# Performance work log

Hardware: AMD Instinct MI355X
Metric: run time of the kernel (lower is better)

Reference implementation:

```python
import math
import jax, jax.numpy as jnp
import numpy as np

H, KV, D = 16, 4, 128          # num_heads, num_kv_heads, head_dim
HID = 2048                      # hidden_size
ROPE_BASE = 1e6
EPS = 1e-6


def setup_inputs() -> dict:
    key = jax.random.key(0)
    ks = jax.random.split(key, 3)
    B, S = 2, 2048
    s = 0.02
    return {
        "x": jax.random.normal(ks[0], (B, S, HID), jnp.float32),
        "w_qkv": jax.random.normal(ks[1], (2 * H * D + 2 * KV * D, HID), jnp.float32) * s,
        "w_o": jax.random.normal(ks[2], (HID, H * D), jnp.float32) * s,
        "q_norm_w": jnp.ones((D,), jnp.float32),
        "q_norm_b": jnp.zeros((D,), jnp.float32),
        "k_norm_w": jnp.ones((D,), jnp.float32),
        "k_norm_b": jnp.zeros((D,), jnp.float32),
    }


def _layernorm(x, w, b):
    mu = jnp.mean(x, axis=-1, keepdims=True)
    xc = x - mu
    var = jnp.mean(xc * xc, axis=-1, keepdims=True)
    return xc * jax.lax.rsqrt(var + EPS) * w + b


def _rope(x, cos, sin):
    # x: [B, h, S, D]; cos/sin: [S, D/2]; interleaved real/imag pairs
    xr, xi = x[..., 0::2], x[..., 1::2]
    c, s = cos[None, None], sin[None, None]
    out = jnp.stack([xr * c - xi * s, xr * s + xi * c], axis=-1)
    return out.reshape(x.shape)


def reference(x, w_qkv, w_o, q_norm_w, q_norm_b, k_norm_w, k_norm_b):
    B, S, _ = x.shape
    qkv = x @ w_qkv.T                                  # [B,S,2*H*D+2*KV*D]
    qg, k, v = jnp.split(qkv, [2 * H * D, 2 * H * D + KV * D], axis=-1)
    q, gate = jnp.split(qg, 2, axis=-1)                # [B,S,H*D] each

    q = q.reshape(B, S, H, D).transpose(0, 2, 1, 3)    # [B,H,S,D]
    k = k.reshape(B, S, KV, D).transpose(0, 2, 1, 3)   # [B,KV,S,D]
    v = v.reshape(B, S, KV, D).transpose(0, 2, 1, 3)

    q = _layernorm(q, q_norm_w, q_norm_b)
    k = _layernorm(k, k_norm_w, k_norm_b)

    inv = 1.0 / (ROPE_BASE ** (jnp.arange(0, D, 2, dtype=jnp.float32) / D))
    freqs = jnp.outer(jnp.arange(S, dtype=jnp.float32), inv)  # [S, D/2]
    cos, sin = jnp.cos(freqs), jnp.sin(freqs)
    q = _rope(q, cos, sin)
    k = _rope(k, cos, sin)

    rep = H // KV
    k = jnp.repeat(k, rep, axis=1)                     # [B,H,S,D]
    v = jnp.repeat(v, rep, axis=1)

    scores = jnp.einsum('bhqd,bhkd->bhqk', q, k) / math.sqrt(D)
    causal = jnp.tril(jnp.ones((S, S), bool))
    scores = jnp.where(causal[None, None], scores, -jnp.inf)
    attn = jax.nn.softmax(scores, axis=-1)
    out = jnp.einsum('bhqk,bhkd->bhqd', attn, v)
    out = out.transpose(0, 2, 1, 3).reshape(B, S, H * D)
    out = out * jax.nn.sigmoid(gate)
    return out @ w_o.T
```

## Files before the change

### kernel.cpp

```cpp
#include <hip/hip_runtime.h>
#include <hip/hip_bf16.h>

typedef __bf16 bf16_t;
typedef __bf16 bf16x2 __attribute__((ext_vector_type(2)));
typedef __bf16 bf16x4v __attribute__((ext_vector_type(4)));
typedef __bf16 bf16x8 __attribute__((ext_vector_type(8)));
typedef float f32x4 __attribute__((ext_vector_type(4)));

#define LOG2E 1.4426950408889634f
#define QSCALE (0.08838834764831843f * 1.4426950408889634f)

__global__ __launch_bounds__(256) void cvt_f32_bf16(const float* __restrict__ in,
                                                    bf16_t* __restrict__ out, int n4) {
  int i = blockIdx.x * 256 + threadIdx.x;
  if (i < n4) {
    float4 v = ((const float4*)in)[i];
    bf16x4v o;
    o[0] = (__bf16)v.x; o[1] = (__bf16)v.y; o[2] = (__bf16)v.z; o[3] = (__bf16)v.w;
    *(bf16x4v*)(out + (size_t)i * 4) = o;
  }
}

__global__ __launch_bounds__(256) void rope_tables(float* __restrict__ cosT,
                                                   float* __restrict__ sinT) {
  int idx = blockIdx.x * 256 + threadIdx.x;
  int s = idx >> 6, i = idx & 63;
  float inv = __builtin_amdgcn_exp2f(-(float)i * (19.931568569324174f / 64.0f));
  float f = (float)s * inv;
  cosT[idx] = cosf(f);
  sinT[idx] = sinf(f);
}

template<int MI, int NI, typename OT>
__global__ __launch_bounds__(512) void gemm8p(const bf16_t* __restrict__ A,
                                              const bf16_t* __restrict__ B,
                                              OT* __restrict__ C,
                                              int M, int N, int K) {
  constexpr int BM = MI * 32;
  constexpr int BN = NI * 64;
  constexpr int NA = BM / 64;
  constexpr int NB = BN / 64;
  constexpr int ST = NA + NB;

  __shared__ bf16_t LA[2][BM * 64];
  __shared__ bf16_t LB[2][BN * 64];

  int nb = N / BN;
  int cpx = gridDim.x >> 3;
  int bid = blockIdx.x;
  int swz = (bid & 7) * cpx + (bid >> 3);
  int bm = swz / nb, bn = swz % nb;
  int m0 = bm * BM, n0 = bn * BN;
  int tid = threadIdx.x, lane = tid & 63, wv = tid >> 6;
  int wr = wv >> 2, wc = wv & 3, lr = lane & 15, g = lane >> 4;
  int T = K >> 6;

  auto stageI = [&](int kt, int bi, int s) {
    int k0 = kt << 6;
    if (s < NA) {
      int c = s * 512 + tid;
      int row = c >> 3, lc = (c & 7) ^ (row & 7);
      __builtin_amdgcn_global_load_lds(
          (const __attribute__((address_space(1))) void*)(A + (size_t)(m0 + row) * K + k0 + lc * 8),
          (__attribute__((address_space(3))) void*)&LA[bi][(s * 512 + wv * 64) * 8], 16, 0, 0);
    } else {
      int c = (s - NA) * 512 + tid;
      int row = c >> 3, lc = (c & 7) ^ (row & 7);
      __builtin_amdgcn_global_load_lds(
          (const __attribute__((address_space(1))) void*)(B + (size_t)(n0 + row) * K + k0 + lc * 8),
          (__attribute__((address_space(3))) void*)&LB[bi][((s - NA) * 512 + wv * 64) * 8], 16, 0, 0);
    }
  };

  f32x4 acc[MI][NI];
#pragma unroll
  for (int i = 0; i < MI; i++)
#pragma unroll
    for (int j = 0; j < NI; j++)
#pragma unroll
      for (int r = 0; r < 4; r++) acc[i][j][r] = 0.f;

#pragma unroll
  for (int s = 0; s < ST; s++) stageI(0, 0, s);

  int ofk0 = ((0 + g) ^ (lr & 7)) << 3;
  int ofk1 = ((4 + g) ^ (lr & 7)) << 3;
  int offA = (wr * (MI * 16) + lr) * 64;
  int offB = (wc * (NI * 16) + lr) * 64;

  for (int t = 0; t < T; t++) {
    int bi = t & 1, bo = bi ^ 1;
    const bf16_t* la = LA[bi];
    const bf16_t* lb = LB[bi];
    bool pre = (t + 1 < T);
    if (pre) {
#pragma unroll
      for (int s = 0; s < ST; s++) stageI(t + 1, bo, s);
      if constexpr (ST == 9) asm volatile("s_waitcnt vmcnt(9)" ::: "memory");
      else                   asm volatile("s_waitcnt vmcnt(6)" ::: "memory");
    } else {
      asm volatile("s_waitcnt vmcnt(0)" ::: "memory");
    }
    __builtin_amdgcn_s_barrier();
    asm volatile("" ::: "memory");

    bf16x8 bq0[NI], bq1[NI];
#pragma unroll
    for (int ni = 0; ni < NI; ni++) bq0[ni] = *(const bf16x8*)&lb[offB + ni * 1024 + ofk0];
#pragma unroll
    for (int ni = 0; ni < NI; ni++) bq1[ni] = *(const bf16x8*)&lb[offB + ni * 1024 + ofk1];
#pragma unroll
    for (int q = 0; q < MI / 4; q++) {
      bf16x8 af0[4], af1[4];
#pragma unroll
      for (int i = 0; i < 4; i++)
        af0[i] = *(const bf16x8*)&la[offA + (q * 4 + i) * 1024 + ofk0];
#pragma unroll
      for (int i = 0; i < 4; i++)
#pragma unroll
        for (int ni = 0; ni < NI; ni++)
          acc[q * 4 + i][ni] =
              __builtin_amdgcn_mfma_f32_16x16x32_bf16(af0[i], bq0[ni], acc[q * 4 + i][ni], 0, 0, 0);
#pragma unroll
      for (int i = 0; i < 4; i++)
        af1[i] = *(const bf16x8*)&la[offA + (q * 4 + i) * 1024 + ofk1];
#pragma unroll
      for (int i = 0; i < 4; i++)
#pragma unroll
        for (int ni = 0; ni < NI; ni++)
          acc[q * 4 + i][ni] =
              __builtin_amdgcn_mfma_f32_16x16x32_bf16(af1[i], bq1[ni], acc[q * 4 + i][ni], 0, 0, 0);
    }

    asm volatile("s_waitcnt lgkmcnt(0)" ::: "memory");
    __builtin_amdgcn_s_barrier();
    asm volatile("" ::: "memory");
  }

#pragma unroll
  for (int mi = 0; mi < MI; mi++)
#pragma unroll
    for (int ni = 0; ni < NI; ni++) {
      int m = m0 + wr * (MI * 16) + mi * 16 + g * 4;
      int n = n0 + wc * (NI * 16) + ni * 16 + lr;
#pragma unroll
      for (int r = 0; r < 4; r++) C[(size_t)(m + r) * N + n] = (OT)acc[mi][ni][r];
    }
}

__global__ __launch_bounds__(256) void ln_rope(const bf16_t* __restrict__ qkv,
                                               const float* __restrict__ qw, const float* __restrict__ qb,
                                               const float* __restrict__ kw, const float* __restrict__ kb,
                                               const float* __restrict__ cosT, const float* __restrict__ sinT,
                                               bf16_t* __restrict__ Qr, bf16_t* __restrict__ Kr) {
  int row = blockIdx.x;
  int b = row >> 11, s = row & 2047;
  int lane = threadIdx.x & 63, wv = threadIdx.x >> 6;
  float c = cosT[(s << 6) + lane], sn = sinT[(s << 6) + lane];
  const bf16_t* base = qkv + (size_t)row * 5120;
#pragma unroll
  for (int i = 0; i < 5; i++) {
    int head = wv * 5 + i;
    bool isq = head < 16;
    int off = isq ? (head << 7) : (4096 + ((head - 16) << 7));
    bf16x2 xv = *(const bf16x2*)(base + off + (lane << 1));
    float x0f = (float)xv[0], x1f = (float)xv[1];
    float sum = x0f + x1f;
#pragma unroll
    for (int m = 1; m < 64; m <<= 1) sum += __shfl_xor(sum, m);
    float mu = sum * 0.0078125f;
    float x0 = x0f - mu, x1 = x1f - mu;
    float vs = x0 * x0 + x1 * x1;
#pragma unroll
    for (int m = 1; m < 64; m <<= 1) vs += __shfl_xor(vs, m);
    float rs = rsqrtf(vs * 0.0078125f + 1e-6f);
    const float* w = isq ? qw : kw;
    const float* bb = isq ? qb : kb;
    float y0 = x0 * rs * w[lane << 1] + bb[lane << 1];
    float y1 = x1 * rs * w[(lane << 1) + 1] + bb[(lane << 1) + 1];
    float o0 = y0 * c - y1 * sn;
    float o1 = y0 * sn + y1 * c;
    if (isq) { o0 *= QSCALE; o1 *= QSCALE; }
    bf16x2 ov; ov[0] = (__bf16)o0; ov[1] = (__bf16)o1;
    size_t dst = isq ? ((((size_t)(b * 16 + head)) * 2048 + s) * 128 + (lane << 1))
                     : ((((size_t)(b * 4 + (head - 16))) * 2048 + s) * 128 + (lane << 1));
    *(bf16x2*)((isq ? Qr : Kr) + dst) = ov;
  }
}

__global__ __launch_bounds__(256) void vtrans(const bf16_t* __restrict__ qkv,
                                              bf16_t* __restrict__ Vt) {
  int bid = blockIdx.x;
  int sb = bid & 63, kv = (bid >> 6) & 3, b = bid >> 8;
  int s0 = sb << 5;
  __shared__ bf16_t T[128 * 33];
  int tid = threadIdx.x;
#pragma unroll
  for (int i = 0; i < 16; i++) {
    int idx = i * 256 + tid;
    int r = idx >> 7, d = idx & 127;
    T[d * 33 + r] = qkv[((size_t)(b * 2048 + s0 + r)) * 5120 + 4608 + (kv << 7) + d];
  }
  __syncthreads();
#pragma unroll
  for (int j = 0; j < 16; j++) {
    int idx = j * 256 + tid;
    int d = idx >> 5, sc = idx & 31;
    Vt[(((size_t)(b * 4 + kv)) * 128 + d) * 2048 + s0 + sc] = T[d * 33 + sc];
  }
}

__global__ __launch_bounds__(256, 3) void attn(const bf16_t* __restrict__ Qr,
                                               const bf16_t* __restrict__ Kr,
                                               const bf16_t* __restrict__ Vt,
                                               const bf16_t* __restrict__ qkv,
                                               bf16_t* __restrict__ ag) {
  __shared__ bf16_t Ks[2][32 * 128];
  __shared__ bf16_t Vs[2][128 * 32];
  int bid = blockIdx.x;
  int hb = bid & 31;
  int h = hb & 15, b = hb >> 4;
  int pr = bid >> 5;
  int kvh = h >> 2;
  int tid = threadIdx.x, lane = tid & 63, wv = tid >> 6;
  int lr = lane & 15, g = lane >> 4;
  int r0base = ((lr >> 2) << 3) + (lr & 3);

  const bf16_t* Kg = Kr + ((size_t)(b * 4 + kvh)) * 2048 * 128;
  const bf16_t* Vg = Vt + ((size_t)(b * 4 + kvh)) * 128 * 2048;

  auto stage = [&](int buf, int kv0) {
#pragma unroll
    for (int i = 0; i < 2; i++) {
      int c = i * 256 + tid;
      int row = c >> 4, lc = (c & 15) ^ (row & 15);
      __builtin_amdgcn_global_load_lds(
          (const __attribute__((address_space(1))) void*)(Kg + (size_t)(kv0 + row) * 128 + lc * 8),
          (__attribute__((address_space(3))) void*)&Ks[buf][c * 8], 16, 0, 0);
    }
#pragma unroll
    for (int i = 0; i < 2; i++) {
      int c = i * 256 + tid;
      int d = c >> 2, cv = (c & 3) ^ ((d >> 1) & 3);
      __builtin_amdgcn_global_load_lds(
          (const __attribute__((address_space(1))) void*)(Vg + (size_t)d * 2048 + kv0 + cv * 8),
          (__attribute__((address_space(3))) void*)&Vs[buf][c * 8], 16, 0, 0);
    }
  };

  auto sm = [&](const f32x4& s0, const f32x4& s1, int qrow, int kvabs, bool dia,
                float& mrun, float& lsp, bf16x8& pb, f32x4 (&oac)[8]) {
    float tt[8];
#pragma unroll
    for (int r = 0; r < 4; r++) { tt[r] = s0[r]; tt[4 + r] = s1[r]; }
    if (dia) {
#pragma unroll
      for (int r = 0; r < 4; r++) {
        if (kvabs + r > qrow)     tt[r]     = -1e30f;
        if (kvabs + 4 + r > qrow) tt[4 + r] = -1e30f;
      }
    }
    float lm = fmaxf(fmaxf(fmaxf(tt[0], tt[1]), tt[2]),
                     fmaxf(fmaxf(tt[3], tt[4]), fmaxf(fmaxf(tt[5], tt[6]), tt[7])));
    if (__all(lm <= mrun + 8.f)) {
      float ps = 0.f;
#pragma unroll
      for (int i = 0; i < 8; i++) {
        float pv = __builtin_amdgcn_exp2f(tt[i] - mrun);
        pb[i] = (__bf16)pv; ps += pv;
      }
      lsp += ps;
    } else {
      float pm = lm;
      pm = fmaxf(pm, __shfl_xor(pm, 16));
      pm = fmaxf(pm, __shfl_xor(pm, 32));
      float mnew = fmaxf(mrun, pm);
      float corr = __builtin_amdgcn_exp2f(mrun - mnew);
      float ps = 0.f;
#pragma unroll
      for (int i = 0; i < 8; i++) {
        float pv = __builtin_amdgcn_exp2f(tt[i] - mnew);
        pb[i] = (__bf16)pv; ps += pv;
      }
      lsp = lsp * corr + ps;
      mrun = mnew;
#pragma unroll
      for (int dt = 0; dt < 8; dt++)
#pragma unroll
        for (int r = 0; r < 4; r++) oac[dt][r] *= corr;
    }
  };

  for (int phase = 0; phase < 2; phase++) {
    int qb = phase ? (31 - pr) : pr;
    int qw0 = qb << 6;
    int qw = qw0 + (wv << 4);
    int qrow = qw + lr;
    int qmax = qw + 15;
    int nt = (qb + 1) << 1;

    const bf16_t* Qg = Qr + (((size_t)(b * 16 + h)) * 2048 + qrow) * 128;
    bf16x8 qf[4];
#pragma unroll
    for (int ds = 0; ds < 4; ds++) qf[ds] = *(const bf16x8*)(Qg + ds * 32 + g * 8);

    f32x4 oa[8];
#pragma unroll
    for (int i = 0; i < 8; i++)
#pragma unroll
      for (int r = 0; r < 4; r++) oa[i][r] = 0.f;
    float mrun = -1e30f, lsp = 0.f;

    stage(0, 0);
    for (int t = 0; t < nt; t++) {
      int cur = t & 1;
      if (t + 1 < nt) {
        stage(cur ^ 1, (t + 1) << 5);
        asm volatile("s_waitcnt vmcnt(4)" ::: "memory");
      } else {
        asm volatile("s_waitcnt vmcnt(0)" ::: "memory");
      }
      __builtin_amdgcn_s_barrier();
      asm volatile("" ::: "memory");
      int kvb = t << 5;
      if (kvb <= qmax) {
        const bf16_t* kb = Ks[cur];
        const bf16_t* vb = Vs[cur];
        int ra = r0base, rb2 = r0base + 4;
        bf16x8 a0[4], a1[4];
#pragma unroll
        for (int ds = 0; ds < 4; ds++) {
          a0[ds] = *(const bf16x8*)&kb[ra * 128 + (((ds * 4 + g) ^ (ra & 15)) << 3)];
          a1[ds] = *(const bf16x8*)&kb[rb2 * 128 + (((ds * 4 + g) ^ (rb2 & 15)) << 3)];
        }
        f32x4 s0, s1;
#pragma unroll
        for (int r = 0; r < 4; r++) { s0[r] = 0.f; s1[r] = 0.f; }
        __builtin_amdgcn_s_setprio(1);
#pragma unroll
        for (int ds = 0; ds < 4; ds++) {
          s0 = __builtin_amdgcn_mfma_f32_16x16x32_bf16(a0[ds], qf[ds], s0, 0, 0, 0);
          s1 = __builtin_amdgcn_mfma_f32_16x16x32_bf16(a1[ds], qf[ds], s1, 0, 0, 0);
        }
        __builtin_amdgcn_s_setprio(0);
        int kvabs = kvb + (g << 3);
        bool dia = (kvb + 31 > qw);
        bf16x8 pb;
        sm(s0, s1, qrow, kvabs, dia, mrun, lsp, pb, oa);
        __builtin_amdgcn_s_setprio(1);
#pragma unroll
        for (int dt = 0; dt < 8; dt++) {
          int d = dt * 16 + lr;
          bf16x8 va = *(const bf16x8*)&vb[d * 32 + ((g ^ ((d >> 1) & 3)) << 3)];
          oa[dt] = __builtin_amdgcn_mfma_f32_16x16x32_bf16(va, pb, oa[dt], 0, 0, 0);
        }
        __builtin_amdgcn_s_setprio(0);
      }
      asm volatile("s_waitcnt lgkmcnt(0)" ::: "memory");
      __builtin_amdgcn_s_barrier();
      asm volatile("" ::: "memory");
    }

    float ls = lsp + __shfl_xor(lsp, 16);
    ls += __shfl_xor(ls, 32);
    float invl = __builtin_amdgcn_rcpf(ls);

    size_t ob = ((size_t)b * 2048 + qrow) * 2048 + (h << 7);
    size_t gb = ((size_t)b * 2048 + qrow) * 5120 + 2048 + (h << 7);
#pragma unroll
    for (int dt = 0; dt < 8; dt++) {
      int d = dt * 16 + (g << 2);
      bf16x4v gt = *(const bf16x4v*)(qkv + gb + d);
      bf16x4v o;
      o[0] = (__bf16)(oa[dt][0] * invl * __builtin_amdgcn_rcpf(1.f + __builtin_amdgcn_exp2f(-(float)gt[0] * LOG2E)));
      o[1] = (__bf16)(oa[dt][1] * invl * __builtin_amdgcn_rcpf(1.f + __builtin_amdgcn_exp2f(-(float)gt[1] * LOG2E)));
      o[2] = (__bf16)(oa[dt][2] * invl * __builtin_amdgcn_rcpf(1.f + __builtin_amdgcn_exp2f(-(float)gt[2] * LOG2E)));
      o[3] = (__bf16)(oa[dt][3] * invl * __builtin_amdgcn_rcpf(1.f + __builtin_amdgcn_exp2f(-(float)gt[3] * LOG2E)));
      *(bf16x4v*)(ag + ob + d) = o;
    }
  }
}

extern "C" void kernel_launch(void* const* d_in, const int* in_sizes, int n_in,
                              void* d_out, int out_size, void* d_ws, size_t ws_size,
                              hipStream_t stream) {
  const float* x    = (const float*)d_in[0];
  const float* wqkv = (const float*)d_in[1];
  const float* wo   = (const float*)d_in[2];
  const float* qnw  = (const float*)d_in[3];
  const float* qnb  = (const float*)d_in[4];
  const float* knw  = (const float*)d_in[5];
  const float* knb  = (const float*)d_in[6];
  float* out = (float*)d_out;

  char* p = (char*)d_ws;
  bf16_t* xb  = (bf16_t*)p;
  bf16_t* ag  = xb;
  p += (size_t)16777216;
  bf16_t* wqb = (bf16_t*)p;
  bf16_t* Qr  = wqb;
  p += (size_t)20971520;
  bf16_t* wob = (bf16_t*)p; p += (size_t)8388608;
  bf16_t* qkv = (bf16_t*)p; p += (size_t)41943040;
  bf16_t* Kr  = (bf16_t*)p; p += (size_t)4194304;
  bf16_t* Vt  = (bf16_t*)p; p += (size_t)4194304;
  float* cosT = (float*)p;  p += (size_t)524288;
  float* sinT = (float*)p;  p += (size_t)524288;

  cvt_f32_bf16<<<8192, 256, 0, stream>>>(x, xb, 2097152);
  cvt_f32_bf16<<<10240, 256, 0, stream>>>(wqkv, wqb, 2621440);
  cvt_f32_bf16<<<4096, 256, 0, stream>>>(wo, wob, 1048576);
  rope_tables<<<512, 256, 0, stream>>>(cosT, sinT);

  gemm8p<8, 5, bf16_t><<<256, 512, 0, stream>>>(xb, wqb, qkv, 4096, 5120, 2048);

  ln_rope<<<4096, 256, 0, stream>>>(qkv, qnw, qnb, knw, knb, cosT, sinT, Qr, Kr);
  vtrans<<<512, 256, 0, stream>>>(qkv, Vt);

  attn<<<512, 256, 0, stream>>>(Qr, Kr, Vt, qkv, ag);

  gemm8p<4, 4, float><<<256, 512, 0, stream>>>(ag, wob, out, 4096, 2048, 2048);
}
```

Measured before the change: 236.5 us.

## Merge conversion kernels, vectorize LN-RoPE, and cut one barrier per pipeline iteration

```diff
diff --git a/kernel.cpp b/kernel.cpp
--- a/kernel.cpp
+++ b/kernel.cpp
@@ -10,15 +10,18 @@
 #define LOG2E 1.4426950408889634f
 #define QSCALE (0.08838834764831843f * 1.4426950408889634f)
 
-__global__ __launch_bounds__(256) void cvt_f32_bf16(const float* __restrict__ in,
-                                                    bf16_t* __restrict__ out, int n4) {
+__global__ __launch_bounds__(256) void cvt_all(const float* __restrict__ x, bf16_t* __restrict__ xb,
+                                               const float* __restrict__ wq, bf16_t* __restrict__ wqb,
+                                               const float* __restrict__ wo, bf16_t* __restrict__ wob) {
   int i = blockIdx.x * 256 + threadIdx.x;
-  if (i < n4) {
-    float4 v = ((const float4*)in)[i];
-    bf16x4v o;
-    o[0] = (__bf16)v.x; o[1] = (__bf16)v.y; o[2] = (__bf16)v.z; o[3] = (__bf16)v.w;
-    *(bf16x4v*)(out + (size_t)i * 4) = o;
-  }
+  const float* in; bf16_t* out; int idx;
+  if (i < 2097152)      { in = x;  out = xb;  idx = i; }
+  else if (i < 4718592) { in = wq; out = wqb; idx = i - 2097152; }
+  else                  { in = wo; out = wob; idx = i - 4718592; }
+  float4 v = ((const float4*)in)[idx];
+  bf16x4v o;
+  o[0] = (__bf16)v.x; o[1] = (__bf16)v.y; o[2] = (__bf16)v.z; o[3] = (__bf16)v.w;
+  *(bf16x4v*)(out + (size_t)idx * 4) = o;
 }
 
 __global__ __launch_bounds__(256) void rope_tables(float* __restrict__ cosT,
@@ -82,6 +85,9 @@
 
 #pragma unroll
   for (int s = 0; s < ST; s++) stageI(0, 0, s);
+  asm volatile("s_waitcnt vmcnt(0)" ::: "memory");
+  __builtin_amdgcn_s_barrier();
+  asm volatile("" ::: "memory");
 
   int ofk0 = ((0 + g) ^ (lr & 7)) << 3;
   int ofk1 = ((4 + g) ^ (lr & 7)) << 3;
@@ -96,13 +102,7 @@
     if (pre) {
 #pragma unroll
       for (int s = 0; s < ST; s++) stageI(t + 1, bo, s);
-      if constexpr (ST == 9) asm volatile("s_waitcnt vmcnt(9)" ::: "memory");
-      else                   asm volatile("s_waitcnt vmcnt(6)" ::: "memory");
-    } else {
-      asm volatile("s_waitcnt vmcnt(0)" ::: "memory");
-    }
-    __builtin_amdgcn_s_barrier();
-    asm volatile("" ::: "memory");
+    }
 
     bf16x8 bq0[NI], bq1[NI];
 #pragma unroll
@@ -132,9 +132,11 @@
               __builtin_amdgcn_mfma_f32_16x16x32_bf16(af1[i], bq1[ni], acc[q * 4 + i][ni], 0, 0, 0);
     }
 
-    asm volatile("s_waitcnt lgkmcnt(0)" ::: "memory");
-    __builtin_amdgcn_s_barrier();
-    asm volatile("" ::: "memory");
+    if (pre) {
+      asm volatile("s_waitcnt vmcnt(0) lgkmcnt(0)" ::: "memory");
+      __builtin_amdgcn_s_barrier();
+      asm volatile("" ::: "memory");
+    }
   }
 
 #pragma unroll
@@ -155,36 +157,57 @@
                                                bf16_t* __restrict__ Qr, bf16_t* __restrict__ Kr) {
   int row = blockIdx.x;
   int b = row >> 11, s = row & 2047;
-  int lane = threadIdx.x & 63, wv = threadIdx.x >> 6;
-  float c = cosT[(s << 6) + lane], sn = sinT[(s << 6) + lane];
+  int tid = threadIdx.x, gi = tid >> 4, li = tid & 15;
   const bf16_t* base = qkv + (size_t)row * 5120;
-#pragma unroll
-  for (int i = 0; i < 5; i++) {
-    int head = wv * 5 + i;
-    bool isq = head < 16;
+  float4 c4 = *(const float4*)(cosT + (s << 6) + (li << 2));
+  float4 s4 = *(const float4*)(sinT + (s << 6) + (li << 2));
+#pragma unroll
+  for (int it = 0; it < 2; it++) {
+    int head;
+    if (it == 0) head = gi;
+    else { if (gi >= 4) break; head = 16 + gi; }
+    bool isq = (it == 0);
     int off = isq ? (head << 7) : (4096 + ((head - 16) << 7));
-    bf16x2 xv = *(const bf16x2*)(base + off + (lane << 1));
-    float x0f = (float)xv[0], x1f = (float)xv[1];
-    float sum = x0f + x1f;
-#pragma unroll
-    for (int m = 1; m < 64; m <<= 1) sum += __shfl_xor(sum, m);
+    bf16x8 xv = *(const bf16x8*)(base + off + (li << 3));
+    float xf[8];
+#pragma unroll
+    for (int j = 0; j < 8; j++) xf[j] = (float)xv[j];
+    float sum = 0.f;
+#pragma unroll
+    for (int j = 0; j < 8; j++) sum += xf[j];
+#pragma unroll
+    for (int m = 1; m < 16; m <<= 1) sum += __shfl_xor(sum, m);
     float mu = sum * 0.0078125f;
-    float x0 = x0f - mu, x1 = x1f - mu;
-    float vs = x0 * x0 + x1 * x1;
-#pragma unroll
-    for (int m = 1; m < 64; m <<= 1) vs += __shfl_xor(vs, m);
+    float vs = 0.f;
+#pragma unroll
+    for (int j = 0; j < 8; j++) { xf[j] -= mu; vs += xf[j] * xf[j]; }
+#pragma unroll
+    for (int m = 1; m < 16; m <<= 1) vs += __shfl_xor(vs, m);
     float rs = rsqrtf(vs * 0.0078125f + 1e-6f);
     const float* w = isq ? qw : kw;
     const float* bb = isq ? qb : kb;
-    float y0 = x0 * rs * w[lane << 1] + bb[lane << 1];
-    float y1 = x1 * rs * w[(lane << 1) + 1] + bb[(lane << 1) + 1];
-    float o0 = y0 * c - y1 * sn;
-    float o1 = y0 * sn + y1 * c;
-    if (isq) { o0 *= QSCALE; o1 *= QSCALE; }
-    bf16x2 ov; ov[0] = (__bf16)o0; ov[1] = (__bf16)o1;
-    size_t dst = isq ? ((((size_t)(b * 16 + head)) * 2048 + s) * 128 + (lane << 1))
-                     : ((((size_t)(b * 4 + (head - 16))) * 2048 + s) * 128 + (lane << 1));
-    *(bf16x2*)((isq ? Qr : Kr) + dst) = ov;
+    float4 w0 = *(const float4*)(w + (li << 3));
+    float4 w1 = *(const float4*)(w + (li << 3) + 4);
+    float4 b0 = *(const float4*)(bb + (li << 3));
+    float4 b1 = *(const float4*)(bb + (li << 3) + 4);
+    float y[8];
+    y[0] = xf[0] * rs * w0.x + b0.x; y[1] = xf[1] * rs * w0.y + b0.y;
+    y[2] = xf[2] * rs * w0.z + b0.z; y[3] = xf[3] * rs * w0.w + b0.w;
+    y[4] = xf[4] * rs * w1.x + b1.x; y[5] = xf[5] * rs * w1.y + b1.y;
+    y[6] = xf[6] * rs * w1.z + b1.z; y[7] = xf[7] * rs * w1.w + b1.w;
+    float cc[4] = { c4.x, c4.y, c4.z, c4.w };
+    float ss[4] = { s4.x, s4.y, s4.z, s4.w };
+    bf16x8 ov;
+#pragma unroll
+    for (int p = 0; p < 4; p++) {
+      float o0 = y[2 * p] * cc[p] - y[2 * p + 1] * ss[p];
+      float o1 = y[2 * p] * ss[p] + y[2 * p + 1] * cc[p];
+      if (isq) { o0 *= QSCALE; o1 *= QSCALE; }
+      ov[2 * p] = (__bf16)o0; ov[2 * p + 1] = (__bf16)o1;
+    }
+    size_t dst = isq ? ((((size_t)(b * 16 + head)) * 2048 + s) * 128 + (li << 3))
+                     : ((((size_t)(b * 4 + (head - 16))) * 2048 + s) * 128 + (li << 3));
+    *(bf16x8*)((isq ? Qr : Kr) + dst) = ov;
   }
 }
 
@@ -312,16 +335,12 @@
     float mrun = -1e30f, lsp = 0.f;
 
     stage(0, 0);
+    asm volatile("s_waitcnt vmcnt(0)" ::: "memory");
+    __builtin_amdgcn_s_barrier();
+    asm volatile("" ::: "memory");
     for (int t = 0; t < nt; t++) {
       int cur = t & 1;
-      if (t + 1 < nt) {
-        stage(cur ^ 1, (t + 1) << 5);
-        asm volatile("s_waitcnt vmcnt(4)" ::: "memory");
-      } else {
-        asm volatile("s_waitcnt vmcnt(0)" ::: "memory");
-      }
-      __builtin_amdgcn_s_barrier();
-      asm volatile("" ::: "memory");
+      if (t + 1 < nt) stage(cur ^ 1, (t + 1) << 5);
       int kvb = t << 5;
       if (kvb <= qmax) {
         const bf16_t* kb = Ks[cur];
@@ -356,7 +375,7 @@
         }
         __builtin_amdgcn_s_setprio(0);
       }
-      asm volatile("s_waitcnt lgkmcnt(0)" ::: "memory");
+      asm volatile("s_waitcnt vmcnt(0) lgkmcnt(0)" ::: "memory");
       __builtin_amdgcn_s_barrier();
       asm volatile("" ::: "memory");
     }
@@ -407,9 +426,7 @@
   float* cosT = (float*)p;  p += (size_t)524288;
   float* sinT = (float*)p;  p += (size_t)524288;
 
-  cvt_f32_bf16<<<8192, 256, 0, stream>>>(x, xb, 2097152);
-  cvt_f32_bf16<<<10240, 256, 0, stream>>>(wqkv, wqb, 2621440);
-  cvt_f32_bf16<<<4096, 256, 0, stream>>>(wo, wob, 1048576);
+  cvt_all<<<22528, 256, 0, stream>>>(x, xb, wqkv, wqb, wo, wob);
   rope_tables<<<512, 256, 0, stream>>>(cosT, sinT);
 
   gemm8p<8, 5, bf16_t><<<256, 512, 0, stream>>>(xb, wqb, qkv, 4096, 5120, 2048);
```

New measurement: 232.7 us. Within noise of the previous version (-1.6%).
